# Performance work log

Measured on AMD Instinct MI355X. Metric: run time of the kernel, lower is better.

The kernel has to match this reference:

```python
import jax, jax.numpy as jnp
import numpy as np

B, S, D, H, HS = 4, 2048, 1024, 16, 64
DFF = 4 * D
EPS = 1e-5


def setup_inputs() -> dict:
    key = jax.random.key(0)
    ks = jax.random.split(key, 16)
    std = 0.02
    return {
        "x": jax.random.normal(ks[0], (B, S, D), jnp.float32),
        "Wq": jax.random.normal(ks[1], (H, D, HS), jnp.float32) * std,
        "bq": jnp.zeros((H, HS), jnp.float32),
        "Wk": jax.random.normal(ks[2], (H, D, HS), jnp.float32) * std,
        "bk": jnp.zeros((H, HS), jnp.float32),
        "Wv": jax.random.normal(ks[3], (H, D, HS), jnp.float32) * std,
        "bv": jnp.zeros((H, HS), jnp.float32),
        "Wp": jax.random.normal(ks[4], (D, D), jnp.float32) * std,
        "bp": jnp.zeros((D,), jnp.float32),
        "ln1_w": jnp.ones((D,), jnp.float32),
        "ln1_b": jnp.zeros((D,), jnp.float32),
        "ln2_w": jnp.ones((D,), jnp.float32),
        "ln2_b": jnp.zeros((D,), jnp.float32),
        "W1": jax.random.normal(ks[5], (D, DFF), jnp.float32) * std,
        "b1": jnp.zeros((DFF,), jnp.float32),
        "W2": jax.random.normal(ks[6], (DFF, D), jnp.float32) * std,
        "b2": jnp.zeros((D,), jnp.float32),
    }


def _layernorm(x, w, b):
    mu = jnp.mean(x, axis=-1, keepdims=True)
    var = jnp.mean(jnp.square(x - mu), axis=-1, keepdims=True)
    return (x - mu) * jax.lax.rsqrt(var + EPS) * w + b


def _block(x, Wq, bq, Wk, bk, Wv, bv, Wp, bp, ln1_w, ln1_b, ln2_w, ln2_b, W1, b1, W2, b2):
    seq = x.shape[1]
    xn = _layernorm(x, ln1_w, ln1_b)
    # batched per-head projections: [B,H,S,HS]
    q = jnp.einsum('bsd,hdk->bhsk', xn, Wq) + bq[:, None, :]
    k = jnp.einsum('bsd,hdk->bhsk', xn, Wk) + bk[:, None, :]
    v = jnp.einsum('bsd,hdk->bhsk', xn, Wv) + bv[:, None, :]
    scores = jnp.einsum('bhsk,bhtk->bhst', q, k)
    mask = jnp.tril(jnp.ones((seq, seq), bool))
    # original: masked_fill(-inf) then divide by sqrt(head_size) -> equivalent
    scores = jnp.where(mask, scores / jnp.sqrt(jnp.float32(HS)), -jnp.inf)
    attn = jax.nn.softmax(scores, axis=-1)
    out = jnp.einsum('bhst,bhtk->bhsk', attn, v)
    out = out.transpose(0, 2, 1, 3).reshape(x.shape[0], seq, H * HS)
    att = out @ Wp + bp
    x = x + att
    xn2 = _layernorm(x, ln2_w, ln2_b)
    h = jax.nn.gelu(xn2 @ W1 + b1, approximate=False)  # torch nn.GELU default = exact
    ffn = h @ W2 + b2
    return x + ffn


def reference(x, Wq, bq, Wk, bk, Wv, bv, Wp, bp, ln1_w, ln1_b, ln2_w, ln2_b, W1, b1, W2, b2):
    out = _block(x, Wq, bq, Wk, bk, Wv, bv, Wp, bp, ln1_w, ln1_b, ln2_w, ln2_b, W1, b1, W2, b2)
    return out
```

## Files before the change

### kernel.cpp

```cpp
#include <hip/hip_runtime.h>
#include <hip/hip_bf16.h>

#define D_MODEL 1024
#define SEQ 2048
#define NH 16
#define HSZ 64
#define DFF_ 4096

typedef __attribute__((ext_vector_type(8))) short short8;
typedef __attribute__((ext_vector_type(4))) short short4v;
typedef __attribute__((ext_vector_type(4))) float f32x4;

static __device__ __forceinline__ short f2bf(float f) {
  unsigned u = __builtin_bit_cast(unsigned, f);
  u = u + 0x7fffu + ((u >> 16) & 1u);
  return (short)(u >> 16);
}

static __device__ __forceinline__ unsigned packbf2(float a, float b) {
  return (unsigned)(unsigned short)f2bf(a) | ((unsigned)(unsigned short)f2bf(b) << 16);
}

static __device__ __forceinline__ f32x4 mfma16(short8 a, short8 b, f32x4 c) {
  return __builtin_amdgcn_mfma_f32_16x16x32_bf16(a, b, c, 0, 0, 0);
}

static __device__ __forceinline__ void gld16(const short* g, short* l) {
  __builtin_amdgcn_global_load_lds((const __attribute__((address_space(1))) void*)g,
                                   (__attribute__((address_space(3))) void*)l, 16, 0, 0);
}

__global__ void transpose_qkv_kernel(const float* __restrict__ Wq, const float* __restrict__ Wk,
                                     const float* __restrict__ Wv, short* __restrict__ dst) {
  __shared__ float tile[32][33];
  const int z = blockIdx.z;
  const int which = z >> 4, hh = z & 15;
  const float* src = (which == 0 ? Wq : which == 1 ? Wk : Wv) + (long)hh * (D_MODEL * HSZ);
  const int c0 = blockIdx.x * 32, r0 = blockIdx.y * 32;
  const int tx = threadIdx.x, ty = threadIdx.y;
#pragma unroll
  for (int i = 0; i < 4; ++i)
    tile[ty + 8 * i][tx] = src[(long)(r0 + ty + 8 * i) * HSZ + c0 + tx];
  __syncthreads();
#pragma unroll
  for (int i = 0; i < 4; ++i)
    dst[((long)which * 1024 + hh * 64 + c0 + ty + 8 * i) * D_MODEL + r0 + tx] =
        f2bf(tile[tx][ty + 8 * i]);
}

__global__ void transpose_gen_kernel(const float* __restrict__ src, short* __restrict__ dst,
                                     int R, int C) {
  __shared__ float tile[32][33];
  const int c0 = blockIdx.x * 32, r0 = blockIdx.y * 32;
  const int tx = threadIdx.x, ty = threadIdx.y;
#pragma unroll
  for (int i = 0; i < 4; ++i)
    tile[ty + 8 * i][tx] = src[(long)(r0 + ty + 8 * i) * C + c0 + tx];
  __syncthreads();
#pragma unroll
  for (int i = 0; i < 4; ++i)
    dst[(long)(c0 + ty + 8 * i) * R + r0 + tx] = f2bf(tile[tx][ty + 8 * i]);
}

__global__ void v_transpose_kernel(const short* __restrict__ vb, short* __restrict__ vt) {
  __shared__ short tile[64 * 72];
  const int bh = blockIdx.y;
  const int t0 = blockIdx.x * 64;
  const long base = (long)bh * SEQ * HSZ;
  const int tid = threadIdx.x;
  const int r = tid >> 3, c = (tid & 7) * 8;
#pragma unroll
  for (int it = 0; it < 2; ++it) {
    const int rr = r + it * 32;
    *(short8*)&tile[rr * 72 + c] = *(const short8*)(vb + base + (long)(t0 + rr) * HSZ + c);
  }
  __syncthreads();
#pragma unroll
  for (int it = 0; it < 2; ++it) {
    const int rr = r + it * 32;
    short8 o;
#pragma unroll
    for (int u = 0; u < 8; ++u) o[u] = tile[(c + u) * 72 + rr];
    *(short8*)(vt + base + (long)rr * SEQ + t0 + c) = o;
  }
}

__global__ void ln_kernel(const float* __restrict__ x, const float* __restrict__ w,
                          const float* __restrict__ b, short* __restrict__ out) {
  const int row = blockIdx.x;
  const float* xr = x + (size_t)row * D_MODEL;
  const int t = threadIdx.x;
  float4 v = *(const float4*)(xr + t * 4);
  float s = v.x + v.y + v.z + v.w;
  float s2 = v.x * v.x + v.y * v.y + v.z * v.z + v.w * v.w;
#pragma unroll
  for (int o = 1; o < 64; o <<= 1) {
    s += __shfl_xor(s, o, 64);
    s2 += __shfl_xor(s2, o, 64);
  }
  __shared__ float ps[8];
  const int lane = t & 63, wid = t >> 6;
  if (lane == 0) { ps[wid] = s; ps[wid + 4] = s2; }
  __syncthreads();
  s = ps[0] + ps[1] + ps[2] + ps[3];
  s2 = ps[4] + ps[5] + ps[6] + ps[7];
  const float mu = s * (1.0f / D_MODEL);
  const float var = s2 * (1.0f / D_MODEL) - mu * mu;
  const float rs = rsqrtf(var + 1e-5f);
  float4 wv = *(const float4*)(w + t * 4);
  float4 bv = *(const float4*)(b + t * 4);
  short4v o4;
  o4[0] = f2bf((v.x - mu) * rs * wv.x + bv.x);
  o4[1] = f2bf((v.y - mu) * rs * wv.y + bv.y);
  o4[2] = f2bf((v.z - mu) * rs * wv.z + bv.z);
  o4[3] = f2bf((v.w - mu) * rs * wv.w + bv.w);
  *(short4v*)(out + (size_t)row * D_MODEL + t * 4) = o4;
}

template <int MODE>
__global__ __launch_bounds__(512, 2) void gemm_kernel(
    const short* __restrict__ A, const short* __restrict__ Bt, const int K,
    const int gridX, const float* __restrict__ c0, const float* __restrict__ c1,
    const float* __restrict__ c2, const float* __restrict__ res,
    void* __restrict__ o0, void* __restrict__ o1, void* __restrict__ o2) {
  __shared__ short As[2][128 * 64];
  __shared__ short Bs[2][256 * 64];
  const int nwg = (int)gridDim.x;
  const int bid0 = (int)blockIdx.x;
  const int bid = (bid0 & 7) * (nwg >> 3) + (bid0 >> 3);
  const int bx = bid % gridX, by = bid / gridX;
  const long r0 = (long)by * 128;
  const long n0 = (long)bx * 256;
  const int tid = threadIdx.x;
  const int lane = tid & 63, wid = tid >> 6;
  const int wm = wid >> 2, wn = wid & 3;
  const int l16 = lane & 15, lg = lane >> 4;

  long offA[2], offB[4];
#pragma unroll
  for (int i = 0; i < 2; ++i) {
    const int c = tid + i * 512;
    const int row = c >> 3, slot = c & 7;
    offA[i] = (long)(r0 + row) * K + ((slot ^ (row & 7)) << 3);
  }
#pragma unroll
  for (int i = 0; i < 4; ++i) {
    const int c = tid + i * 512;
    const int row = c >> 3, slot = c & 7;
    offB[i] = (long)(n0 + row) * K + ((slot ^ (row & 7)) << 3);
  }

  f32x4 acc[4][4];
#pragma unroll
  for (int m = 0; m < 4; ++m)
#pragma unroll
    for (int n = 0; n < 4; ++n) {
      f32x4 z = {0.f, 0.f, 0.f, 0.f};
      acc[m][n] = z;
    }

  const int x7 = l16 & 7;
  const int sw0 = (lg ^ x7) * 8, sw1 = ((4 + lg) ^ x7) * 8;

#define STAGE_T(kt, buf)                                                      \
  {                                                                           \
    _Pragma("unroll") for (int i = 0; i < 2; ++i)                             \
        gld16(A + offA[i] + (kt), &As[buf][(tid + i * 512) * 8]);             \
    _Pragma("unroll") for (int i = 0; i < 4; ++i)                             \
        gld16(Bt + offB[i] + (kt), &Bs[buf][(tid + i * 512) * 8]);            \
  }

  const int NT = K >> 6;
  STAGE_T(0, 0);
  __syncthreads();

  for (int t = 0; t < NT; ++t) {
    const int p = t & 1;
    if (t + 1 < NT) STAGE_T((t + 1) << 6, p ^ 1);
    const short* Ap = As[p];
    const short* Bp = Bs[p];
#pragma unroll
    for (int mq = 0; mq < 2; ++mq)
#pragma unroll
      for (int nq = 0; nq < 2; ++nq) {
        short8 af[2][2], bf[2][2];
#pragma unroll
        for (int m = 0; m < 2; ++m) {
          const int r = wm * 64 + mq * 32 + m * 16 + l16;
          af[m][0] = *(const short8*)&Ap[r * 64 + sw0];
          af[m][1] = *(const short8*)&Ap[r * 64 + sw1];
        }
#pragma unroll
        for (int n = 0; n < 2; ++n) {
          const int r = wn * 64 + nq * 32 + n * 16 + l16;
          bf[n][0] = *(const short8*)&Bp[r * 64 + sw0];
          bf[n][1] = *(const short8*)&Bp[r * 64 + sw1];
        }
        __builtin_amdgcn_s_setprio(1);
#pragma unroll
        for (int m = 0; m < 2; ++m)
#pragma unroll
          for (int n = 0; n < 2; ++n) {
            acc[mq * 2 + m][nq * 2 + n] =
                mfma16(af[m][0], bf[n][0], acc[mq * 2 + m][nq * 2 + n]);
            acc[mq * 2 + m][nq * 2 + n] =
                mfma16(af[m][1], bf[n][1], acc[mq * 2 + m][nq * 2 + n]);
          }
        __builtin_amdgcn_s_setprio(0);
      }
    __syncthreads();
  }
#undef STAGE_T

#pragma unroll
  for (int m = 0; m < 4; ++m) {
    const long rowb = r0 + wm * 64 + m * 16 + lg * 4;
#pragma unroll
    for (int n = 0; n < 4; ++n) {
      const long col = n0 + wn * 64 + n * 16 + l16;
#pragma unroll
      for (int j = 0; j < 4; ++j) {
        float val = acc[m][n][j];
        const long rr = rowb + j;
        if (MODE == 0) {
          const int c10 = (int)col & 1023;
          const int which = (int)col >> 10;
          const float* bb = which == 0 ? c0 : which == 1 ? c1 : c2;
          short* oo = (short*)(which == 0 ? o0 : which == 1 ? o1 : o2);
          val += bb[c10];
          const long bidx = rr >> 11, sidx = rr & 2047;
          const int h = c10 >> 6, hs = c10 & 63;
          oo[(((bidx * NH) + h) * SEQ + sidx) * HSZ + hs] = f2bf(val);
        } else if (MODE == 1) {
          val += c0[col] + res[rr * D_MODEL + col];
          ((float*)o0)[rr * D_MODEL + col] = val;
        } else if (MODE == 2) {
          val += c0[col];
          const float g = 0.5f * val * (1.0f + erff(val * 0.70710678118654752f));
          ((short*)o0)[rr * DFF_ + col] = f2bf(g);
        } else {
          val += c0[col] + res[rr * D_MODEL + col];
          ((float*)o0)[rr * D_MODEL + col] = val;
        }
      }
    }
  }
}

#define SM_SCALE 0.18033688011112042f

__global__ void attn_kernel(const short* __restrict__ q, const short* __restrict__ k,
                            const short* __restrict__ vt, short* __restrict__ att) {
  const int qt = (SEQ / 128 - 1) - (int)blockIdx.y;
  const int bh = blockIdx.x;
  const int b = bh >> 4, h = bh & 15;
  const int tid = threadIdx.x;
  const int lane = tid & 63, wq = tid >> 6;
  const int l16 = lane & 15, lg = lane >> 4;
  const long base = (long)bh * SEQ * HSZ;

  __shared__ short Ks[64 * 64];
  __shared__ short Vts[64 * 64];
  __shared__ short Ps[4 * 32 * 72];
  short* Psw = &Ps[wq * 32 * 72];

  const int R0 = qt * 128 + wq * 32;

  short8 qf[2][2];
#pragma unroll
  for (int qn = 0; qn < 2; ++qn)
#pragma unroll
    for (int kk = 0; kk < 2; ++kk)
      qf[qn][kk] =
          *(const short8*)(q + base + (long)(R0 + qn * 16 + l16) * HSZ + kk * 32 + lg * 8);

  float m_[2] = {-INFINITY, -INFINITY};
  float l_[2] = {0.f, 0.f};
  f32x4 oacc[2][4];
#pragma unroll
  for (int qn = 0; qn < 2; ++qn)
#pragma unroll
    for (int hf = 0; hf < 4; ++hf) {
      f32x4 z = {0.f, 0.f, 0.f, 0.f};
      oacc[qn][hf] = z;
    }

  const int srow = tid >> 3, wg = tid & 7;
  const int swc = (wg ^ (srow & 7)) * 8;
  const int x7 = l16 & 7;
  const int rc0 = (lg ^ x7) * 8, rc1 = ((4 + lg) ^ x7) * 8;
  const int tend = (qt + 1) * 128;

  for (int t0 = 0; t0 < tend; t0 += 64) {
    __syncthreads();
#pragma unroll
    for (int it = 0; it < 2; ++it) {
      const int r = srow + it * 32;
      const short8 kv = *(const short8*)(k + base + (long)(t0 + r) * HSZ + wg * 8);
      const short8 vv = *(const short8*)(vt + base + (long)r * SEQ + t0 + wg * 8);
      *(short8*)&Ks[r * 64 + swc] = kv;
      *(short8*)&Vts[r * 64 + swc] = vv;
    }
    __syncthreads();

    if (t0 <= R0 + 31) {
      f32x4 sf[4][2];
#pragma unroll
      for (int tt = 0; tt < 4; ++tt)
#pragma unroll
        for (int qn = 0; qn < 2; ++qn) {
          f32x4 z = {0.f, 0.f, 0.f, 0.f};
          sf[tt][qn] = z;
        }
      __builtin_amdgcn_s_setprio(1);
#pragma unroll
      for (int kk = 0; kk < 2; ++kk)
#pragma unroll
        for (int tt = 0; tt < 4; ++tt) {
          short8 kf = *(const short8*)&Ks[(tt * 16 + l16) * 64 + (kk ? rc1 : rc0)];
#pragma unroll
          for (int qn = 0; qn < 2; ++qn) sf[tt][qn] = mfma16(kf, qf[qn][kk], sf[tt][qn]);
        }
      __builtin_amdgcn_s_setprio(0);

      const bool domask = (t0 + 63 > R0);
      const int tb = t0 + lg * 4;
#pragma unroll
      for (int tt = 0; tt < 4; ++tt)
#pragma unroll
        for (int qn = 0; qn < 2; ++qn) {
          const int qg = R0 + qn * 16 + l16;
#pragma unroll
          for (int j = 0; j < 4; ++j) {
            float s = sf[tt][qn][j] * SM_SCALE;
            if (domask && (tb + tt * 16 + j > qg)) s = -INFINITY;
            sf[tt][qn][j] = s;
          }
        }

      float mx[2];
#pragma unroll
      for (int qn = 0; qn < 2; ++qn) {
        float m0 = sf[0][qn][0];
#pragma unroll
        for (int tt = 0; tt < 4; ++tt)
#pragma unroll
          for (int j = 0; j < 4; ++j) m0 = fmaxf(m0, sf[tt][qn][j]);
        m0 = fmaxf(m0, __shfl_xor(m0, 16, 64));
        m0 = fmaxf(m0, __shfl_xor(m0, 32, 64));
        mx[qn] = m0;
      }
      const int ok = (mx[0] <= m_[0] + 8.f) && (mx[1] <= m_[1] + 8.f);
      if (!__all(ok)) {
#pragma unroll
        for (int qn = 0; qn < 2; ++qn) {
          const float mnew = fmaxf(m_[qn], mx[qn]);
          const float rc = exp2f(m_[qn] - mnew);
          m_[qn] = mnew;
          l_[qn] *= rc;
#pragma unroll
          for (int hf = 0; hf < 4; ++hf)
#pragma unroll
            for (int j = 0; j < 4; ++j) oacc[qn][hf][j] *= rc;
        }
      }
#pragma unroll
      for (int qn = 0; qn < 2; ++qn) {
        float sum = 0.f;
#pragma unroll
        for (int tt = 0; tt < 4; ++tt)
#pragma unroll
          for (int j = 0; j < 4; ++j) {
            const float p = exp2f(sf[tt][qn][j] - m_[qn]);
            sf[tt][qn][j] = p;
            sum += p;
          }
        l_[qn] += sum;
      }

#pragma unroll
      for (int qn = 0; qn < 2; ++qn)
#pragma unroll
        for (int tt = 0; tt < 4; ++tt) {
          const int ro = (qn * 16 + l16) * 72 + tt * 16 + lg * 4;
          *(unsigned*)&Psw[ro] = packbf2(sf[tt][qn][0], sf[tt][qn][1]);
          *(unsigned*)&Psw[ro + 2] = packbf2(sf[tt][qn][2], sf[tt][qn][3]);
        }

      __builtin_amdgcn_s_setprio(1);
#pragma unroll
      for (int kk = 0; kk < 2; ++kk) {
        short8 pa[2];
#pragma unroll
        for (int qn = 0; qn < 2; ++qn)
          pa[qn] = *(const short8*)&Psw[(qn * 16 + l16) * 72 + kk * 32 + lg * 8];
#pragma unroll
        for (int hf = 0; hf < 4; ++hf) {
          short8 vf = *(const short8*)&Vts[(hf * 16 + l16) * 64 + (kk ? rc1 : rc0)];
#pragma unroll
          for (int qn = 0; qn < 2; ++qn)
            oacc[qn][hf] = mfma16(vf, pa[qn], oacc[qn][hf]);
        }
      }
      __builtin_amdgcn_s_setprio(0);
    }
  }

#pragma unroll
  for (int qn = 0; qn < 2; ++qn) {
    float lt = l_[qn];
    lt += __shfl_xor(lt, 16, 64);
    lt += __shfl_xor(lt, 32, 64);
    const float inv = 1.0f / lt;
    const long row = R0 + qn * 16 + l16;
#pragma unroll
    for (int hf = 0; hf < 4; ++hf) {
      short4v o4;
#pragma unroll
      for (int j = 0; j < 4; ++j) o4[j] = f2bf(oacc[qn][hf][j] * inv);
      *(short4v*)(att + ((long)b * SEQ + row) * D_MODEL + h * HSZ + hf * 16 + lg * 4) = o4;
    }
  }
}

extern "C" void kernel_launch(void* const* d_in, const int* in_sizes, int n_in,
                              void* d_out, int out_size, void* d_ws, size_t ws_size,
                              hipStream_t stream) {
  const float* x = (const float*)d_in[0];
  const float* Wq = (const float*)d_in[1];
  const float* bq = (const float*)d_in[2];
  const float* Wk = (const float*)d_in[3];
  const float* bk = (const float*)d_in[4];
  const float* Wv = (const float*)d_in[5];
  const float* bv = (const float*)d_in[6];
  const float* Wp = (const float*)d_in[7];
  const float* bp = (const float*)d_in[8];
  const float* g1 = (const float*)d_in[9];
  const float* be1 = (const float*)d_in[10];
  const float* g2 = (const float*)d_in[11];
  const float* be2 = (const float*)d_in[12];
  const float* W1 = (const float*)d_in[13];
  const float* b1 = (const float*)d_in[14];
  const float* W2 = (const float*)d_in[15];
  const float* b2 = (const float*)d_in[16];
  float* out = (float*)d_out;
  char* ws = (char*)d_ws;

  if (ws_size < 209715200ull) return;

  short* WqkvT = (short*)(ws + 0);
  short* WpT = (short*)(ws + 6291456);
  short* W1T = (short*)(ws + 8388608);
  short* W2T = (short*)(ws + 16777216);
  short* xn = (short*)(ws + 25165824);
  short* vt = (short*)(ws + 25165824);
  short* qb = (short*)(ws + 41943040);
  short* kb = (short*)(ws + 58720256);
  short* vb = (short*)(ws + 75497472);
  short* att = (short*)(ws + 92274688);
  float* x1 = (float*)(ws + 109051904);
  short* hb = (short*)(ws + 142606336);

  dim3 tb(32, 8);
  transpose_qkv_kernel<<<dim3(2, 32, 48), tb, 0, stream>>>(Wq, Wk, Wv, WqkvT);
  transpose_gen_kernel<<<dim3(32, 32), tb, 0, stream>>>(Wp, WpT, 1024, 1024);
  transpose_gen_kernel<<<dim3(128, 32), tb, 0, stream>>>(W1, W1T, 1024, 4096);
  transpose_gen_kernel<<<dim3(32, 128), tb, 0, stream>>>(W2, W2T, 4096, 1024);
  ln_kernel<<<8192, 256, 0, stream>>>(x, g1, be1, xn);
  gemm_kernel<0><<<768, 512, 0, stream>>>(xn, WqkvT, 1024, 12, bq, bk, bv, nullptr, qb,
                                          kb, vb);
  v_transpose_kernel<<<dim3(32, 64), 256, 0, stream>>>(vb, vt);
  attn_kernel<<<dim3(64, 16), 256, 0, stream>>>(qb, kb, vt, att);
  gemm_kernel<1><<<256, 512, 0, stream>>>(att, WpT, 1024, 4, bp, nullptr, nullptr, x, x1,
                                          nullptr, nullptr);
  ln_kernel<<<8192, 256, 0, stream>>>(x1, g2, be2, xn);
  gemm_kernel<2><<<1024, 512, 0, stream>>>(xn, W1T, 1024, 16, b1, nullptr, nullptr,
                                           nullptr, hb, nullptr, nullptr);
  gemm_kernel<3><<<256, 512, 0, stream>>>(hb, W2T, 4096, 4, b2, nullptr, nullptr, x1, out,
                                          nullptr, nullptr);
}
```

Before: 481.7 us.

## Triple-buffer GEMM LDS tiles with explicit vmcnt waits and 2D grid

The bf16 MFMA GEMM moves from double to triple LDS buffering. Global loads are issued two k-tiles ahead and tracked with explicit s_waitcnt vmcnt instead of a full __syncthreads per iteration. B fragments are now loaded once per k-tile and reused across both mq halves. The XCD-aware block index swizzle is replaced by a plain 2D grid. The extra buffer grows LDS to about 144KB per block, which likely allows only one 512-thread block per CU despite launch_bounds(512,2), and dropping the swizzle may hurt L2 locality.

```diff
diff --git a/kernel.cpp b/kernel.cpp
--- a/kernel.cpp
+++ b/kernel.cpp
@@ -120,17 +120,13 @@
 template <int MODE>
 __global__ __launch_bounds__(512, 2) void gemm_kernel(
     const short* __restrict__ A, const short* __restrict__ Bt, const int K,
-    const int gridX, const float* __restrict__ c0, const float* __restrict__ c1,
+    const float* __restrict__ c0, const float* __restrict__ c1,
     const float* __restrict__ c2, const float* __restrict__ res,
     void* __restrict__ o0, void* __restrict__ o1, void* __restrict__ o2) {
-  __shared__ short As[2][128 * 64];
-  __shared__ short Bs[2][256 * 64];
-  const int nwg = (int)gridDim.x;
-  const int bid0 = (int)blockIdx.x;
-  const int bid = (bid0 & 7) * (nwg >> 3) + (bid0 >> 3);
-  const int bx = bid % gridX, by = bid / gridX;
-  const long r0 = (long)by * 128;
-  const long n0 = (long)bx * 256;
+  __shared__ short As[3][128 * 64];
+  __shared__ short Bs[3][256 * 64];
+  const long r0 = (long)blockIdx.y * 128;
+  const long n0 = (long)blockIdx.x * 256;
   const int tid = threadIdx.x;
   const int lane = tid & 63, wid = tid >> 6;
   const int wm = wid >> 2, wn = wid & 3;
@@ -172,49 +168,51 @@
 
   const int NT = K >> 6;
   STAGE_T(0, 0);
-  __syncthreads();
+  STAGE_T(64, 1);
 
   for (int t = 0; t < NT; ++t) {
-    const int p = t & 1;
-    if (t + 1 < NT) STAGE_T((t + 1) << 6, p ^ 1);
-    const short* Ap = As[p];
-    const short* Bp = Bs[p];
-#pragma unroll
-    for (int mq = 0; mq < 2; ++mq)
-#pragma unroll
-      for (int nq = 0; nq < 2; ++nq) {
-        short8 af[2][2], bf[2][2];
-#pragma unroll
-        for (int m = 0; m < 2; ++m) {
-          const int r = wm * 64 + mq * 32 + m * 16 + l16;
-          af[m][0] = *(const short8*)&Ap[r * 64 + sw0];
-          af[m][1] = *(const short8*)&Ap[r * 64 + sw1];
-        }
-#pragma unroll
-        for (int n = 0; n < 2; ++n) {
-          const int r = wn * 64 + nq * 32 + n * 16 + l16;
-          bf[n][0] = *(const short8*)&Bp[r * 64 + sw0];
-          bf[n][1] = *(const short8*)&Bp[r * 64 + sw1];
-        }
-        __builtin_amdgcn_s_setprio(1);
-#pragma unroll
-        for (int m = 0; m < 2; ++m)
-#pragma unroll
-          for (int n = 0; n < 2; ++n) {
-            acc[mq * 2 + m][nq * 2 + n] =
-                mfma16(af[m][0], bf[n][0], acc[mq * 2 + m][nq * 2 + n]);
-            acc[mq * 2 + m][nq * 2 + n] =
-                mfma16(af[m][1], bf[n][1], acc[mq * 2 + m][nq * 2 + n]);
-          }
-        __builtin_amdgcn_s_setprio(0);
-      }
-    __syncthreads();
+    if (t + 1 < NT)
+      asm volatile("s_waitcnt vmcnt(6)" ::: "memory");
+    else
+      asm volatile("s_waitcnt vmcnt(0)" ::: "memory");
+    __builtin_amdgcn_s_barrier();
+    if (t + 2 < NT) STAGE_T((t + 2) << 6, (t + 2) % 3);
+
+    const short* Ap = As[t % 3];
+    const short* Bp = Bs[t % 3];
+    short8 bf[4][2];
+#pragma unroll
+    for (int n = 0; n < 4; ++n) {
+      const int r = (wn * 64 + n * 16 + l16) * 64;
+      bf[n][0] = *(const short8*)&Bp[r + sw0];
+      bf[n][1] = *(const short8*)&Bp[r + sw1];
+    }
+#pragma unroll
+    for (int mq = 0; mq < 2; ++mq) {
+      short8 af[2][2];
+#pragma unroll
+      for (int m = 0; m < 2; ++m) {
+        const int r = (wm * 64 + mq * 32 + m * 16 + l16) * 64;
+        af[m][0] = *(const short8*)&Ap[r + sw0];
+        af[m][1] = *(const short8*)&Ap[r + sw1];
+      }
+      __builtin_amdgcn_s_setprio(1);
+#pragma unroll
+      for (int m = 0; m < 2; ++m)
+#pragma unroll
+        for (int n = 0; n < 4; ++n) {
+          acc[mq * 2 + m][n] = mfma16(af[m][0], bf[n][0], acc[mq * 2 + m][n]);
+          acc[mq * 2 + m][n] = mfma16(af[m][1], bf[n][1], acc[mq * 2 + m][n]);
+        }
+      __builtin_amdgcn_s_setprio(0);
+    }
+    __builtin_amdgcn_s_barrier();
   }
 #undef STAGE_T
 
 #pragma unroll
   for (int m = 0; m < 4; ++m) {
-    const long rowb = r0 + wm * 64 + m * 16 + lg * 4;
+    const long rowb = r0 + wm * 64 + (m >> 1) * 32 + (m & 1) * 16 + lg * 4;
 #pragma unroll
     for (int n = 0; n < 4; ++n) {
       const long col = n0 + wn * 64 + n * 16 + l16;
@@ -467,15 +465,15 @@
   transpose_gen_kernel<<<dim3(128, 32), tb, 0, stream>>>(W1, W1T, 1024, 4096);
   transpose_gen_kernel<<<dim3(32, 128), tb, 0, stream>>>(W2, W2T, 4096, 1024);
   ln_kernel<<<8192, 256, 0, stream>>>(x, g1, be1, xn);
-  gemm_kernel<0><<<768, 512, 0, stream>>>(xn, WqkvT, 1024, 12, bq, bk, bv, nullptr, qb,
-                                          kb, vb);
+  gemm_kernel<0><<<dim3(12, 64), 512, 0, stream>>>(xn, WqkvT, 1024, bq, bk, bv, nullptr,
+                                                   qb, kb, vb);
   v_transpose_kernel<<<dim3(32, 64), 256, 0, stream>>>(vb, vt);
   attn_kernel<<<dim3(64, 16), 256, 0, stream>>>(qb, kb, vt, att);
-  gemm_kernel<1><<<256, 512, 0, stream>>>(att, WpT, 1024, 4, bp, nullptr, nullptr, x, x1,
-                                          nullptr, nullptr);
+  gemm_kernel<1><<<dim3(4, 64), 512, 0, stream>>>(att, WpT, 1024, bp, nullptr, nullptr, x,
+                                                  x1, nullptr, nullptr);
   ln_kernel<<<8192, 256, 0, stream>>>(x1, g2, be2, xn);
-  gemm_kernel<2><<<1024, 512, 0, stream>>>(xn, W1T, 1024, 16, b1, nullptr, nullptr,
-                                           nullptr, hb, nullptr, nullptr);
-  gemm_kernel<3><<<256, 512, 0, stream>>>(hb, W2T, 4096, 4, b2, nullptr, nullptr, x1, out,
-                                          nullptr, nullptr);
-}
+  gemm_kernel<2><<<dim3(16, 64), 512, 0, stream>>>(xn, W1T, 1024, b1, nullptr, nullptr,
+                                                   nullptr, hb, nullptr, nullptr);
+  gemm_kernel<3><<<dim3(4, 64), 512, 0, stream>>>(hb, W2T, 4096, b2, nullptr, nullptr, x1,
+                                                  out, nullptr, nullptr);
+}
```

New measurement: 485.6 us. No clear change (+0.8%).
